# Optimization experiments

Hardware: AMD Instinct MI355X
Metric: run time of the kernel (lower is better)

The kernel has to match this reference:

```python
import jax, jax.numpy as jnp
import numpy as np

B, S, H, NH = 2, 2048, 1024, 16
DK = H // NH

def setup_inputs() -> dict:
    key = jax.random.key(0)
    ks = jax.random.split(key, 8)
    scale = 0.02
    return {
        "x": jax.random.normal(ks[0], (B, S, H), jnp.float32),
        "mask": jax.random.randint(ks[1], (B, S, S), 0, 2, jnp.int32),
        "alibi": jax.random.normal(ks[2], (1, NH, S, S), jnp.float32),
        "W_q": jax.random.normal(ks[3], (H, H), jnp.float32) * scale,
        "b_q": jnp.zeros((H,), jnp.float32),
        "W_k": jax.random.normal(ks[4], (H, H), jnp.float32) * scale,
        "b_k": jnp.zeros((H,), jnp.float32),
        "W_v": jax.random.normal(ks[5], (H, H), jnp.float32) * scale,
        "b_v": jnp.zeros((H,), jnp.float32),
        "W_o": jax.random.normal(ks[6], (H, H), jnp.float32) * scale,
        "b_o": jnp.zeros((H,), jnp.float32),
    }

def reference(x, mask, alibi, W_q, b_q, W_k, b_k, W_v, b_v, W_o, b_o):
    b, s, h = x.shape
    def split_heads(t):  # [B,S,H] -> [B,NH,S,DK]
        return t.reshape(b, s, NH, DK).transpose(0, 2, 1, 3)
    q = split_heads(x @ W_q + b_q)
    k = split_heads(x @ W_k + b_k)
    v = split_heads(x @ W_v + b_v)
    scores = jnp.einsum("bhqd,bhkd->bhqk", q, k) / jnp.sqrt(jnp.float32(DK))
    scores = scores + alibi
    scores = jnp.where(mask[:, None, :, :] == 0, jnp.float32(-1e9), scores)
    probs = jax.nn.softmax(scores, axis=-1)  # dropout is identity in eval
    ctx = jnp.einsum("bhqk,bhkd->bhqd", probs, v)
    ctx = ctx.transpose(0, 2, 1, 3).reshape(b, s, h)
    return ctx @ W_o + b_o
```

## Files before the change

### kernel.cpp

```cpp
#include <hip/hip_runtime.h>
#include <hip/hip_bf16.h>


#define S_LEN 2048
#define H_DIM 1024
#define N_HEADS 16

typedef __bf16 bf16x8 __attribute__((ext_vector_type(8)));
typedef __bf16 bf16x4 __attribute__((ext_vector_type(4)));
typedef float f32x4 __attribute__((ext_vector_type(4)));

using gvoid = __attribute__((address_space(1))) void;
using svoid = __attribute__((address_space(3))) void;

static __device__ __forceinline__ f32x4 mfma16(bf16x8 a, bf16x8 b, f32x4 c) {
  return __builtin_amdgcn_mfma_f32_16x16x32_bf16(a, b, c, 0, 0, 0);
}

template <int NCH, int NW>
static __device__ __forceinline__ void stage64(const __bf16* g, int rstride,
                                               __bf16* lds, int wid, int lane) {
#pragma unroll
  for (int i = 0; i < NCH / NW; ++i) {
    int chunk = i * NW + wid;
    int u = chunk * 64 + lane;
    int r = u >> 3, s = u & 7;
    const __bf16* src = g + (size_t)r * rstride + ((s ^ (r & 7)) << 3);
    __builtin_amdgcn_global_load_lds((const gvoid*)src,
                                     (svoid*)(lds + chunk * 512), 16, 0, 0);
  }
}

static __device__ __forceinline__ bf16x8 read_frag(const __bf16* lds, int r,
                                                   int slot) {
  return *(const bf16x8*)(lds + r * 64 + ((slot ^ (r & 7)) << 3));
}

__global__ __launch_bounds__(256) void k_convert_x(const float* __restrict__ x,
                                                   __bf16* __restrict__ xb) {
  size_t idx = ((size_t)blockIdx.x * 256 + threadIdx.x) * 8;
  float4 a = *(const float4*)(x + idx);
  float4 b = *(const float4*)(x + idx + 4);
  bf16x8 o;
  o[0] = (__bf16)a.x; o[1] = (__bf16)a.y; o[2] = (__bf16)a.z; o[3] = (__bf16)a.w;
  o[4] = (__bf16)b.x; o[5] = (__bf16)b.y; o[6] = (__bf16)b.z; o[7] = (__bf16)b.w;
  *(bf16x8*)(xb + idx) = o;
}

__global__ __launch_bounds__(256) void k_transpose_w(
    const float* __restrict__ w0, const float* __restrict__ w1,
    const float* __restrict__ w2, const float* __restrict__ w3,
    __bf16* __restrict__ wt) {
  __shared__ float t[64][65];
  int z = blockIdx.z;
  const float* W = (z == 0) ? w0 : (z == 1) ? w1 : (z == 2) ? w2 : w3;
  __bf16* O = wt + (size_t)z * H_DIM * H_DIM;
  int k0 = blockIdx.x * 64, n0 = blockIdx.y * 64;
  int tid = threadIdx.x;
  {
    int r = tid >> 4, c4 = tid & 15;
#pragma unroll
    for (int i = 0; i < 4; ++i) {
      float4 v = *(const float4*)(W + (size_t)(k0 + r + i * 16) * H_DIM + n0 + c4 * 4);
      t[r + i * 16][c4 * 4 + 0] = v.x;
      t[r + i * 16][c4 * 4 + 1] = v.y;
      t[r + i * 16][c4 * 4 + 2] = v.z;
      t[r + i * 16][c4 * 4 + 3] = v.w;
    }
  }
  __syncthreads();
  {
    int nn = tid >> 2, js = (tid & 3) * 16;
    bf16x8 o0, o1;
#pragma unroll
    for (int j = 0; j < 8; ++j) {
      o0[j] = (__bf16)t[js + j][nn];
      o1[j] = (__bf16)t[js + 8 + j][nn];
    }
    __bf16* dst = O + (size_t)(n0 + nn) * H_DIM + k0 + js;
    *(bf16x8*)dst = o0;
    *(bf16x8*)(dst + 8) = o1;
  }
}

__global__ __launch_bounds__(256) void k_transpose_v(const __bf16* __restrict__ V,
                                                     __bf16* __restrict__ VT) {
  __shared__ __bf16 t[64][65];
  int bh = blockIdx.y;
  int s0 = blockIdx.x * 64;
  const __bf16* Vb = V + (size_t)bh * S_LEN * 64;
  int tid = threadIdx.x;
#pragma unroll
  for (int i = 0; i < 2; ++i) {
    int u = i * 256 + tid;
    int r = u >> 3, c8 = u & 7;
    bf16x8 v = *(const bf16x8*)(Vb + (size_t)(s0 + r) * 64 + c8 * 8);
#pragma unroll
    for (int j = 0; j < 8; ++j) t[r][c8 * 8 + j] = v[j];
  }
  __syncthreads();
  int d = tid >> 2, js = (tid & 3) * 16;
  bf16x8 o0, o1;
#pragma unroll
  for (int j = 0; j < 8; ++j) {
    o0[j] = t[js + j][d];
    o1[j] = t[js + 8 + j][d];
  }
  __bf16* dst = VT + (size_t)bh * 64 * S_LEN + (size_t)d * S_LEN + s0 + js;
  *(bf16x8*)dst = o0;
  *(bf16x8*)(dst + 8) = o1;
}

__global__ __launch_bounds__(256) void k_pack_mask(
    const int* __restrict__ m, unsigned long long* __restrict__ out) {
  size_t idx = (size_t)blockIdx.x * 256 + threadIdx.x;
  unsigned long long b = __ballot(m[idx] != 0);
  if ((threadIdx.x & 63) == 0) out[idx >> 6] = b;
}

template <int MODE>
__global__ __launch_bounds__(256) void k_gemm(
    const __bf16* __restrict__ A, const __bf16* __restrict__ B0,
    const __bf16* __restrict__ B1, const __bf16* __restrict__ B2,
    const float* __restrict__ bias0, const float* __restrict__ bias1,
    const float* __restrict__ bias2, __bf16* __restrict__ O0,
    __bf16* __restrict__ O1, __bf16* __restrict__ O2, float* __restrict__ Of) {
  __shared__ alignas(16) __bf16 As[128 * 64];
  __shared__ alignas(16) __bf16 Bs[128 * 64];
  int tid = threadIdx.x, wid = tid >> 6, lane = tid & 63;
  int l15 = lane & 15, lg = lane >> 4;
  int nbase = blockIdx.x * 128, mbase = blockIdx.y * 128;
  const __bf16* Bm;
  const float* bias;
  __bf16* Ob;
  float oscale = 1.0f;
  if (MODE == 0) {
    int z = blockIdx.z;
    Bm = (z == 0) ? B0 : (z == 1) ? B1 : B2;
    bias = (z == 0) ? bias0 : (z == 1) ? bias1 : bias2;
    Ob = (z == 0) ? O0 : (z == 1) ? O1 : O2;
    if (z == 0) oscale = 0.125f;
  } else {
    Bm = B0; bias = bias0; Ob = O0;
  }
  int wrow = wid >> 1, wcol = wid & 1;
  f32x4 zero = {0.f, 0.f, 0.f, 0.f};
  f32x4 acc[4][4];
#pragma unroll
  for (int i = 0; i < 4; ++i)
#pragma unroll
    for (int j = 0; j < 4; ++j) acc[i][j] = zero;

  for (int kb = 0; kb < H_DIM; kb += 64) {
    __syncthreads();
    const __bf16* Abase;
    int arstride;
    if (MODE == 0) {
      Abase = A + (size_t)mbase * H_DIM + kb;
      arstride = H_DIM;
    } else {
      int b = mbase >> 11, q0 = mbase & 2047, head = kb >> 6;
      Abase = A + ((size_t)(b * N_HEADS + head) * S_LEN + q0) * 64;
      arstride = 64;
    }
    stage64<16, 4>(Abase, arstride, As, wid, lane);
    stage64<16, 4>(Bm + (size_t)nbase * H_DIM + kb, H_DIM, Bs, wid, lane);
    __syncthreads();
#pragma unroll
    for (int t = 0; t < 2; ++t) {
      bf16x8 a[4], bfr[4];
#pragma unroll
      for (int i = 0; i < 4; ++i)
        a[i] = read_frag(As, wrow * 64 + i * 16 + l15, t * 4 + lg);
#pragma unroll
      for (int j = 0; j < 4; ++j)
        bfr[j] = read_frag(Bs, wcol * 64 + j * 16 + l15, t * 4 + lg);
#pragma unroll
      for (int i = 0; i < 4; ++i)
#pragma unroll
        for (int j = 0; j < 4; ++j) acc[i][j] = mfma16(a[i], bfr[j], acc[i][j]);
    }
  }
  float bv[4];
#pragma unroll
  for (int j = 0; j < 4; ++j) bv[j] = bias[nbase + wcol * 64 + j * 16 + l15];
#pragma unroll
  for (int i = 0; i < 4; ++i)
#pragma unroll
    for (int j = 0; j < 4; ++j)
#pragma unroll
      for (int r = 0; r < 4; ++r) {
        int m = mbase + wrow * 64 + i * 16 + lg * 4 + r;
        int col = nbase + wcol * 64 + j * 16 + l15;
        float v = (acc[i][j][r] + bv[j]) * oscale;
        if (MODE == 0) {
          size_t off =
              (((size_t)(m >> 11) * N_HEADS + (col >> 6)) * S_LEN + (m & 2047)) * 64 +
              (col & 63);
          Ob[off] = (__bf16)v;
        } else {
          Of[(size_t)m * H_DIM + col] = v;
        }
      }
}

__global__ __launch_bounds__(512) void k_attn(
    const __bf16* __restrict__ Q, const __bf16* __restrict__ K,
    const __bf16* __restrict__ VT, const float* __restrict__ alibi,
    const unsigned long long* __restrict__ maskb, __bf16* __restrict__ ctx) {
  __shared__ alignas(16) __bf16 Ks[2][64 * 64];
  __shared__ alignas(16) __bf16 Vs[2][64 * 64];
  __shared__ alignas(16) __bf16 Ps[8][16 * 72];
  int tid = threadIdx.x, wid = tid >> 6, lane = tid & 63;
  int l15 = lane & 15, lg = lane >> 4;
  int bh = blockIdx.x;
  int b = bh & 1, h = bh >> 1;
  int qbase = blockIdx.y * 128;
  size_t bho = (size_t)(b * N_HEADS + h);
  const __bf16* Qb = Q + bho * S_LEN * 64;
  const __bf16* Kb = K + bho * S_LEN * 64;
  const __bf16* Vb = VT + bho * 64 * S_LEN;
  const int q = qbase + wid * 16 + l15;

  bf16x8 qa[2];
  {
    const __bf16* qrow = Qb + (size_t)q * 64;
    qa[0] = *(const bf16x8*)(qrow + lg * 8);
    qa[1] = *(const bf16x8*)(qrow + 32 + lg * 8);
  }
  float mrun = -__builtin_inff(), lrun = 0.f;
  f32x4 cacc[4];
  f32x4 zero = {0.f, 0.f, 0.f, 0.f};
#pragma unroll
  for (int c = 0; c < 4; ++c) cacc[c] = zero;

  const float* arow = alibi + ((size_t)h * S_LEN + q) * S_LEN + lg * 4;
  const unsigned long long* mrow = maskb + ((size_t)b * S_LEN + q) * (S_LEN / 64);

  f32x4 albP[4];
  unsigned long long mskP;
  auto prefetch = [&](int kt) {
#pragma unroll
    for (int c = 0; c < 4; ++c) albP[c] = *(const f32x4*)(arow + kt + c * 16);
    mskP = mrow[kt >> 6];
  };

  stage64<8, 8>(Kb, 64, Ks[0], wid, lane);
  stage64<8, 8>(Vb, S_LEN, Vs[0], wid, lane);
  prefetch(0);

  for (int t = 0; t < S_LEN / 64; ++t) {
    const int cur = t & 1;
    __syncthreads();
    f32x4 albC[4];
    unsigned long long mskC = mskP;
#pragma unroll
    for (int c = 0; c < 4; ++c) albC[c] = albP[c];
    if (t + 1 < S_LEN / 64) {
      int kn = (t + 1) * 64;
      stage64<8, 8>(Kb + (size_t)kn * 64, 64, Ks[cur ^ 1], wid, lane);
      stage64<8, 8>(Vb + kn, S_LEN, Vs[cur ^ 1], wid, lane);
      prefetch(kn);
    }

    f32x4 sacc[4];
#pragma unroll
    for (int c = 0; c < 4; ++c) sacc[c] = zero;
#pragma unroll
    for (int t2 = 0; t2 < 2; ++t2) {
      bf16x8 kf[4];
#pragma unroll
      for (int c = 0; c < 4; ++c)
        kf[c] = read_frag(Ks[cur], c * 16 + l15, t2 * 4 + lg);
#pragma unroll
      for (int c = 0; c < 4; ++c) sacc[c] = mfma16(kf[c], qa[t2], sacc[c]);
    }

    unsigned long long sh = mskC >> (lg * 4);
    float s[4][4];
    float m16 = -__builtin_inff();
#pragma unroll
    for (int c = 0; c < 4; ++c) {
      unsigned bits = (unsigned)(sh >> (c * 16)) & 0xFu;
#pragma unroll
      for (int r = 0; r < 4; ++r) {
        float a = (bits & (1u << r)) ? albC[c][r] : -1e9f;
        float v = sacc[c][r] + a;
        s[c][r] = v;
        m16 = fmaxf(m16, v);
      }
    }
    m16 = fmaxf(m16, __shfl_xor(m16, 16));
    m16 = fmaxf(m16, __shfl_xor(m16, 32));
    float mn = fmaxf(mrun, m16);
    float scl = __expf(mrun - mn);
    mrun = mn;
    float rs = 0.f;
#pragma unroll
    for (int c = 0; c < 4; ++c)
#pragma unroll
      for (int r = 0; r < 4; ++r) {
        float pe = __expf(s[c][r] - mn);
        s[c][r] = pe;
        rs += pe;
      }
    rs += __shfl_xor(rs, 16);
    rs += __shfl_xor(rs, 32);
    lrun = lrun * scl + rs;
#pragma unroll
    for (int c = 0; c < 4; ++c) {
      f32x4 v = cacc[c];
      v[0] *= scl; v[1] *= scl; v[2] *= scl; v[3] *= scl;
      cacc[c] = v;
    }
#pragma unroll
    for (int c = 0; c < 4; ++c) {
      bf16x4 u;
#pragma unroll
      for (int r = 0; r < 4; ++r) u[r] = (__bf16)s[c][r];
      *(bf16x4*)(&Ps[wid][l15 * 72 + c * 16 + lg * 4]) = u;
    }
#pragma unroll
    for (int t2 = 0; t2 < 2; ++t2) {
      bf16x8 pa = *(const bf16x8*)(&Ps[wid][l15 * 72 + t2 * 32 + lg * 8]);
#pragma unroll
      for (int c = 0; c < 4; ++c) {
        bf16x8 vb = read_frag(Vs[cur], c * 16 + l15, t2 * 4 + lg);
        cacc[c] = mfma16(vb, pa, cacc[c]);
      }
    }
  }
  float inv = 1.0f / lrun;
#pragma unroll
  for (int c = 0; c < 4; ++c) {
    bf16x4 u;
#pragma unroll
    for (int r = 0; r < 4; ++r) u[r] = (__bf16)(cacc[c][r] * inv);
    *(bf16x4*)(ctx + bho * S_LEN * 64 + (size_t)q * 64 + c * 16 + lg * 4) = u;
  }
}

extern "C" void kernel_launch(void* const* d_in, const int* in_sizes, int n_in,
                              void* d_out, int out_size, void* d_ws,
                              size_t ws_size, hipStream_t stream) {
  const float* x = (const float*)d_in[0];
  const int* mask = (const int*)d_in[1];
  const float* alibi = (const float*)d_in[2];
  const float* Wq = (const float*)d_in[3];
  const float* bq = (const float*)d_in[4];
  const float* Wk = (const float*)d_in[5];
  const float* bk = (const float*)d_in[6];
  const float* Wv = (const float*)d_in[7];
  const float* bv = (const float*)d_in[8];
  const float* Wo = (const float*)d_in[9];
  const float* bo = (const float*)d_in[10];
  float* out = (float*)d_out;
  char* ws = (char*)d_ws;

  const size_t MB = 1u << 20;
  __bf16* xb = (__bf16*)(ws);
  __bf16* wt = (__bf16*)(ws + 8 * MB);
  __bf16* Qb = (__bf16*)(ws + 16 * MB);
  __bf16* Kb = (__bf16*)(ws + 24 * MB);
  __bf16* Vb = (__bf16*)(ws + 32 * MB);
  __bf16* VTb = (__bf16*)(ws + 40 * MB);
  __bf16* ctxb = xb;
  __bf16* wtq = wt;
  __bf16* wtk = wt + (1u << 20);
  __bf16* wtv = wt + 2 * (1u << 20);
  __bf16* wto = wt + 3 * (1u << 20);
  unsigned long long* maskb = (unsigned long long*)Vb;

  k_convert_x<<<dim3(2048), 256, 0, stream>>>(x, xb);
  k_transpose_w<<<dim3(16, 16, 4), 256, 0, stream>>>(Wq, Wk, Wv, Wo, wt);
  k_gemm<0><<<dim3(8, 32, 3), 256, 0, stream>>>(xb, wtq, wtk, wtv, bq, bk, bv,
                                                Qb, Kb, Vb, nullptr);
  k_transpose_v<<<dim3(32, 32), 256, 0, stream>>>(Vb, VTb);
  k_pack_mask<<<dim3((2 * S_LEN * S_LEN) / 256), 256, 0, stream>>>(mask, maskb);
  k_attn<<<dim3(32, 16), 512, 0, stream>>>(Qb, Kb, VTb, alibi, maskb, ctxb);
  k_gemm<1><<<dim3(8, 32, 1), 256, 0, stream>>>(ctxb, wto, nullptr, nullptr, bo,
                                                nullptr, nullptr, nullptr,
                                                nullptr, nullptr, out);
}
```

Measured before the change: 249.3 us.

## Restructure attention pipeline with split K/V staging, manual vmcnt waits, lazy rescale

Rewrites the attention loop's load schedule. V for the current tile is now staged into a single LDS buffer, K for the next tile is double-buffered, and the alibi/mask prefetch moves to after the softmax. Barriers become explicit s_barrier calls guarded by hand-counted vmcnt waits and sched_barriers. It also skips rescaling the context accumulator when no row max increased across the wave. The aim is to overlap global loads with compute better and drop redundant multiplies, but the hand-written vmcnt counts depend on how many loads stage64 issues and can race if they are wrong.

```diff
diff --git a/kernel.cpp b/kernel.cpp
--- a/kernel.cpp
+++ b/kernel.cpp
@@ -209,7 +209,7 @@
     const __bf16* __restrict__ VT, const float* __restrict__ alibi,
     const unsigned long long* __restrict__ maskb, __bf16* __restrict__ ctx) {
   __shared__ alignas(16) __bf16 Ks[2][64 * 64];
-  __shared__ alignas(16) __bf16 Vs[2][64 * 64];
+  __shared__ alignas(16) __bf16 Vs[64 * 64];
   __shared__ alignas(16) __bf16 Ps[8][16 * 72];
   int tid = threadIdx.x, wid = tid >> 6, lane = tid & 63;
   int l15 = lane & 15, lg = lane >> 4;
@@ -237,31 +237,26 @@
   const float* arow = alibi + ((size_t)h * S_LEN + q) * S_LEN + lg * 4;
   const unsigned long long* mrow = maskb + ((size_t)b * S_LEN + q) * (S_LEN / 64);
 
+  stage64<8, 8>(Kb, 64, Ks[0], wid, lane);
+  __builtin_amdgcn_sched_barrier(0);
   f32x4 albP[4];
   unsigned long long mskP;
-  auto prefetch = [&](int kt) {
-#pragma unroll
-    for (int c = 0; c < 4; ++c) albP[c] = *(const f32x4*)(arow + kt + c * 16);
-    mskP = mrow[kt >> 6];
-  };
-
-  stage64<8, 8>(Kb, 64, Ks[0], wid, lane);
-  stage64<8, 8>(Vb, S_LEN, Vs[0], wid, lane);
-  prefetch(0);
+#pragma unroll
+  for (int c = 0; c < 4; ++c) albP[c] = *(const f32x4*)(arow + c * 16);
+  mskP = mrow[0];
+  __builtin_amdgcn_sched_barrier(0);
 
   for (int t = 0; t < S_LEN / 64; ++t) {
     const int cur = t & 1;
-    __syncthreads();
-    f32x4 albC[4];
-    unsigned long long mskC = mskP;
-#pragma unroll
-    for (int c = 0; c < 4; ++c) albC[c] = albP[c];
-    if (t + 1 < S_LEN / 64) {
-      int kn = (t + 1) * 64;
-      stage64<8, 8>(Kb + (size_t)kn * 64, 64, Ks[cur ^ 1], wid, lane);
-      stage64<8, 8>(Vb + kn, S_LEN, Vs[cur ^ 1], wid, lane);
-      prefetch(kn);
-    }
+    asm volatile("s_waitcnt vmcnt(5)" ::: "memory");
+    __builtin_amdgcn_sched_barrier(0);
+    __builtin_amdgcn_s_barrier();
+    __builtin_amdgcn_sched_barrier(0);
+    stage64<8, 8>(Vb + (size_t)t * 64, S_LEN, Vs, wid, lane);
+    __builtin_amdgcn_sched_barrier(0);
+    const int kn = (t < S_LEN / 64 - 1 ? t + 1 : t) * 64;
+    stage64<8, 8>(Kb + (size_t)kn * 64, 64, Ks[cur ^ 1], wid, lane);
+    __builtin_amdgcn_sched_barrier(0);
 
     f32x4 sacc[4];
 #pragma unroll
@@ -276,7 +271,7 @@
       for (int c = 0; c < 4; ++c) sacc[c] = mfma16(kf[c], qa[t2], sacc[c]);
     }
 
-    unsigned long long sh = mskC >> (lg * 4);
+    unsigned long long sh = mskP >> (lg * 4);
     float s[4][4];
     float m16 = -__builtin_inff();
 #pragma unroll
@@ -284,7 +279,7 @@
       unsigned bits = (unsigned)(sh >> (c * 16)) & 0xFu;
 #pragma unroll
       for (int r = 0; r < 4; ++r) {
-        float a = (bits & (1u << r)) ? albC[c][r] : -1e9f;
+        float a = (bits & (1u << r)) ? albP[c][r] : -1e9f;
         float v = sacc[c][r] + a;
         s[c][r] = v;
         m16 = fmaxf(m16, v);
@@ -292,6 +287,7 @@
     }
     m16 = fmaxf(m16, __shfl_xor(m16, 16));
     m16 = fmaxf(m16, __shfl_xor(m16, 32));
+    const bool norsc = __all(m16 <= mrun);
     float mn = fmaxf(mrun, m16);
     float scl = __expf(mrun - mn);
     mrun = mn;
@@ -307,11 +303,13 @@
     rs += __shfl_xor(rs, 16);
     rs += __shfl_xor(rs, 32);
     lrun = lrun * scl + rs;
-#pragma unroll
-    for (int c = 0; c < 4; ++c) {
-      f32x4 v = cacc[c];
-      v[0] *= scl; v[1] *= scl; v[2] *= scl; v[3] *= scl;
-      cacc[c] = v;
+    if (!norsc) {
+#pragma unroll
+      for (int c = 0; c < 4; ++c) {
+        f32x4 v = cacc[c];
+        v[0] *= scl; v[1] *= scl; v[2] *= scl; v[3] *= scl;
+        cacc[c] = v;
+      }
     }
 #pragma unroll
     for (int c = 0; c < 4; ++c) {
@@ -320,12 +318,21 @@
       for (int r = 0; r < 4; ++r) u[r] = (__bf16)s[c][r];
       *(bf16x4*)(&Ps[wid][l15 * 72 + c * 16 + lg * 4]) = u;
     }
+    __builtin_amdgcn_sched_barrier(0);
+#pragma unroll
+    for (int c = 0; c < 4; ++c) albP[c] = *(const f32x4*)(arow + kn + c * 16);
+    mskP = mrow[kn >> 6];
+    __builtin_amdgcn_sched_barrier(0);
+    asm volatile("s_waitcnt vmcnt(6)" ::: "memory");
+    __builtin_amdgcn_sched_barrier(0);
+    __builtin_amdgcn_s_barrier();
+    __builtin_amdgcn_sched_barrier(0);
 #pragma unroll
     for (int t2 = 0; t2 < 2; ++t2) {
       bf16x8 pa = *(const bf16x8*)(&Ps[wid][l15 * 72 + t2 * 32 + lg * 8]);
 #pragma unroll
       for (int c = 0; c < 4; ++c) {
-        bf16x8 vb = read_frag(Vs[cur], c * 16 + l15, t2 * 4 + lg);
+        bf16x8 vb = read_frag(Vs, c * 16 + l15, t2 * 4 + lg);
         cacc[c] = mfma16(vb, pa, cacc[c]);
       }
     }
```

Measured after the change: 239.2 us. -4.0%, faster.
